# Performance work log

Measured on AMD Instinct MI355X. Metric: run time of the kernel, lower is better.

The kernel has to match this reference:

```python
import jax, jax.numpy as jnp
import numpy as np

N, E, D = 50000, 600000, 128
EPS = 1e-8
BALL_EPS = 1e-5  # keep norms strictly < 1 for artanh


def _logmap0(x):
    # Poincare ball, c=1: logmap0(x) = artanh(||x||) * x / ||x||
    nrm = jnp.linalg.norm(x, axis=-1, keepdims=True)
    nrm_c = jnp.clip(nrm, EPS, 1.0 - BALL_EPS)
    return jnp.arctanh(nrm_c) * x / nrm_c


def _expmap0(v):
    # Poincare ball, c=1: expmap0(v) = tanh(||v||) * v / ||v||
    nrm = jnp.linalg.norm(v, axis=-1, keepdims=True)
    nrm_c = jnp.maximum(nrm, EPS)
    return jnp.tanh(nrm_c) * v / nrm_c


def setup_inputs() -> dict:
    key = jax.random.key(0)
    ks = jax.random.split(key, 7)
    # node features scaled to lie well inside the unit ball (valid Poincare points)
    x = jax.random.normal(ks[0], (N, D), dtype=jnp.float32) * 0.01
    edge_index = jax.random.randint(ks[1], (2, E), 0, N, dtype=jnp.int32)
    s = 1.0 / np.sqrt(D)
    w_msg1 = jax.random.normal(ks[2], (D, D), dtype=jnp.float32) * s
    w_msg2 = jax.random.normal(ks[3], (D, D), dtype=jnp.float32) * s
    w_upd1 = jax.random.normal(ks[4], (D, D), dtype=jnp.float32) * s
    w_upd2 = jax.random.normal(ks[5], (D, D), dtype=jnp.float32) * s
    b = lambda: jnp.zeros((D,), dtype=jnp.float32)
    return {"x": x, "edge_index": edge_index,
            "w_msg1": w_msg1, "b_msg1": b(), "w_msg2": w_msg2, "b_msg2": b(),
            "w_upd1": w_upd1, "b_upd1": b(), "w_upd2": w_upd2, "b_upd2": b()}


def reference(x, edge_index, w_msg1, b_msg1, w_msg2, b_msg2,
              w_upd1, b_upd1, w_upd2, b_upd2):
    x_t = _logmap0(x)                                  # [N, D]
    row, col = edge_index[0], edge_index[1]            # dst, src
    h = x_t[col]                                       # gather [E, D]
    msgs = jax.nn.relu(h @ w_msg1 + b_msg1) @ w_msg2 + b_msg2   # [E, D]
    # mean aggregation: scatter-add then divide by in-degree
    summed = jax.ops.segment_sum(msgs, row, num_segments=N)      # [N, D]
    count = jax.ops.segment_sum(jnp.ones((E,), dtype=jnp.float32), row, num_segments=N)
    out = summed / (count[:, None] + EPS)
    out = jax.nn.relu(out @ w_upd1 + b_upd1) @ w_upd2 + b_upd2
    return _expmap0(out)
```

## Files before the change

kernel.cpp:

```cpp
#include <hip/hip_runtime.h>
#include <hip/hip_bf16.h>


#define DD 128
#define CAP 64

typedef __attribute__((ext_vector_type(8))) short short8;
typedef __attribute__((ext_vector_type(4))) float f32x4;

__device__ __forceinline__ unsigned short f2bf(float f) {
  unsigned u = __float_as_uint(f);
  u += 0x7fffu + ((u >> 16) & 1u);
  return (unsigned short)(u >> 16);
}
__device__ __forceinline__ float bf2f(short h) {
  return __uint_as_float(((unsigned)(unsigned short)h) << 16);
}

__global__ void k_init(const float* __restrict__ w1, const float* __restrict__ w2,
                       const float* __restrict__ w3, const float* __restrict__ w4,
                       unsigned short* __restrict__ P, int* __restrict__ degv, int N) {
  if (blockIdx.x < 32) {
    int idx = blockIdx.x * 256 + threadIdx.x;
    int m = idx >> 11;
    int id = idx & 2047;
    int f = id >> 6, l = id & 63;
    int cc = f >> 2, s = f & 3, q = l >> 4, n15 = l & 15;
    const float* W = (m == 0) ? w1 : (m == 1) ? w2 : (m == 2) ? w3 : w4;
    const float* wp = W + (s * 32 + q * 8) * DD + cc * 16 + n15;
    unsigned short* op = P + (size_t)m * 16384 + (size_t)id * 8;
#pragma unroll
    for (int j = 0; j < 8; ++j) op[j] = f2bf(wp[j * DD]);
  } else {
    int i = (blockIdx.x - 32) * 256 + threadIdx.x;
    if (i < N) degv[i] = 0;
  }
}

__global__ __launch_bounds__(512) void k_stage1(
    const float* __restrict__ x, const int* __restrict__ ei,
    const unsigned short* __restrict__ Pa, const float* __restrict__ ba,
    const unsigned short* __restrict__ Pb, const float* __restrict__ bb,
    unsigned short* __restrict__ node_msg, int* __restrict__ degv,
    int* __restrict__ ebuf, int N, int E, int nf) {
  __shared__ unsigned short As[64 * 136];
  const int tid = threadIdx.x;

  if (blockIdx.x >= nf) {
    int e0 = (blockIdx.x - nf) * 1024 + tid;
    int e1 = e0 + 512;
    int d0 = 0, d1 = 0, s0i = 0, s1i = 0;
    if (e0 < E) { d0 = ei[e0]; s0i = ei[E + e0]; }
    if (e1 < E) { d1 = ei[e1]; s1i = ei[E + e1]; }
    int p0 = 0, p1 = 0;
    if (e0 < E) p0 = atomicAdd(degv + d0, 1);
    if (e1 < E) p1 = atomicAdd(degv + d1, 1);
    if (e0 < E && p0 < CAP) ebuf[(size_t)d0 * CAP + p0] = s0i;
    if (e1 < E && p1 < CAP) ebuf[(size_t)d1 * CAP + p1] = s1i;
    return;
  }

  const int lane = tid & 63;
  const int wv = tid >> 6;
  const int rt = wv >> 1;
  const int ct = wv & 1;
  const int q = lane >> 4;
  const int n15 = lane & 15;
  const int row0 = blockIdx.x * 64;
  const int g = (wv << 2) | q;

#pragma unroll
  for (int i = 0; i < 2; ++i) {
    const int r = g * 2 + i;
    const int grow = row0 + r;
    f32x4 s0 = {0.f, 0.f, 0.f, 0.f}, s1 = {0.f, 0.f, 0.f, 0.f};
    if (grow < N) {
      const f32x4* p = (const f32x4*)(x + (size_t)grow * DD + n15 * 8);
      s0 = p[0];
      s1 = p[1];
      float ss = s0[0]*s0[0] + s0[1]*s0[1] + s0[2]*s0[2] + s0[3]*s0[3]
               + s1[0]*s1[0] + s1[1]*s1[1] + s1[2]*s1[2] + s1[3]*s1[3];
      ss += __shfl_xor(ss, 1);
      ss += __shfl_xor(ss, 2);
      ss += __shfl_xor(ss, 4);
      ss += __shfl_xor(ss, 8);
      float nrm = sqrtf(ss);
      float nc = fminf(fmaxf(nrm, 1e-8f), 1.0f - 1e-5f);
      float sc = atanhf(nc) / nc;
      s0 *= sc;
      s1 *= sc;
    }
    uint4 pk;
    pk.x = (unsigned)f2bf(s0[0]) | ((unsigned)f2bf(s0[1]) << 16);
    pk.y = (unsigned)f2bf(s0[2]) | ((unsigned)f2bf(s0[3]) << 16);
    pk.z = (unsigned)f2bf(s1[0]) | ((unsigned)f2bf(s1[1]) << 16);
    pk.w = (unsigned)f2bf(s1[2]) | ((unsigned)f2bf(s1[3]) << 16);
    *(uint4*)((unsigned*)As + r * 68 + n15 * 4) = pk;
  }
  __syncthreads();

  float bc[4];
#pragma unroll
  for (int c = 0; c < 4; ++c) bc[c] = ba[ct * 64 + c * 16 + n15];
  f32x4 acc[4];
#pragma unroll
  for (int c = 0; c < 4; ++c) acc[c] = (f32x4){0.f, 0.f, 0.f, 0.f};
  const int abase = (rt * 16 + n15) * 136 + q * 8;
#pragma unroll
  for (int s = 0; s < 4; ++s) {
    short8 a = *(const short8*)&As[abase + s * 32];
#pragma unroll
    for (int c = 0; c < 4; ++c) {
      short8 b = *(const short8*)&Pa[(size_t)(((((ct << 2) | c) << 2) | s) * 64 + lane) * 8];
      acc[c] = __builtin_amdgcn_mfma_f32_16x16x32_bf16(a, b, acc[c], 0, 0, 0);
    }
  }
  __syncthreads();

#pragma unroll
  for (int c = 0; c < 4; ++c)
#pragma unroll
    for (int rr = 0; rr < 4; ++rr) {
      float v = fmaxf(acc[c][rr] + bc[c], 0.f);
      As[(rt * 16 + q * 4 + rr) * 136 + ct * 64 + c * 16 + n15] = f2bf(v);
    }
  __syncthreads();

#pragma unroll
  for (int c = 0; c < 4; ++c) bc[c] = bb[ct * 64 + c * 16 + n15];
#pragma unroll
  for (int c = 0; c < 4; ++c) acc[c] = (f32x4){0.f, 0.f, 0.f, 0.f};
#pragma unroll
  for (int s = 0; s < 4; ++s) {
    short8 a = *(const short8*)&As[abase + s * 32];
#pragma unroll
    for (int c = 0; c < 4; ++c) {
      short8 b = *(const short8*)&Pb[(size_t)(((((ct << 2) | c) << 2) | s) * 64 + lane) * 8];
      acc[c] = __builtin_amdgcn_mfma_f32_16x16x32_bf16(a, b, acc[c], 0, 0, 0);
    }
  }

  __syncthreads();
#pragma unroll
  for (int c = 0; c < 4; ++c)
#pragma unroll
    for (int rr = 0; rr < 4; ++rr)
      As[(rt * 16 + q * 4 + rr) * 136 + ct * 64 + c * 16 + n15] =
          f2bf(acc[c][rr] + bc[c]);
  __syncthreads();
#pragma unroll
  for (int k = 0; k < 2; ++k) {
    int u = tid + k * 512;
    int r = u >> 4, ch = u & 15;
    int grow = row0 + r;
    if (grow < N)
      *(short8*)(node_msg + (size_t)grow * DD + ch * 8) =
          *(const short8*)&As[r * 136 + ch * 8];
  }
}

__global__ __launch_bounds__(512) void k_stage2(
    const unsigned short* __restrict__ node_msg, const int* __restrict__ degv,
    const int* __restrict__ ebuf, const unsigned short* __restrict__ Pa,
    const float* __restrict__ ba, const unsigned short* __restrict__ Pb,
    const float* __restrict__ bb, float* __restrict__ out, int N) {
  __shared__ unsigned short As[64 * 136];
  __shared__ float nrmb[128];
  const int tid = threadIdx.x;
  const int lane = tid & 63;
  const int wv = tid >> 6;
  const int rt = wv >> 1;
  const int ct = wv & 1;
  const int q = lane >> 4;
  const int n15 = lane & 15;
  const int row0 = blockIdx.x * 64;
  const int g = (wv << 2) | q;

  int dpre[2];
#pragma unroll
  for (int i = 0; i < 2; ++i) {
    int grow = row0 + g * 2 + i;
    dpre[i] = (grow < N) ? degv[grow] : 0;
  }

#pragma unroll
  for (int i = 0; i < 2; ++i) {
    const int r = g * 2 + i;
    const int grow = row0 + r;
    f32x4 s0 = {0.f, 0.f, 0.f, 0.f}, s1 = {0.f, 0.f, 0.f, 0.f};
    if (grow < N) {
      const int d = dpre[i];
      const int dl = (d < CAP) ? d : CAP;
      const int* eb = ebuf + (size_t)grow * CAP;
      f32x4 t0 = {0.f, 0.f, 0.f, 0.f}, t1 = {0.f, 0.f, 0.f, 0.f};
      int t = 0;
      for (; t + 3 < dl; t += 4) {
        int4 idx = *(const int4*)(eb + t);
        short8 v0 = *(const short8*)(node_msg + (size_t)idx.x * DD + n15 * 8);
        short8 v1 = *(const short8*)(node_msg + (size_t)idx.y * DD + n15 * 8);
        short8 v2 = *(const short8*)(node_msg + (size_t)idx.z * DD + n15 * 8);
        short8 v3 = *(const short8*)(node_msg + (size_t)idx.w * DD + n15 * 8);
#pragma unroll
        for (int j = 0; j < 4; ++j) {
          s0[j] += bf2f(v0[j]) + bf2f(v1[j]);
          s1[j] += bf2f(v0[j + 4]) + bf2f(v1[j + 4]);
          t0[j] += bf2f(v2[j]) + bf2f(v3[j]);
          t1[j] += bf2f(v2[j + 4]) + bf2f(v3[j + 4]);
        }
      }
      for (; t < dl; ++t) {
        int sa = eb[t];
        short8 va = *(const short8*)(node_msg + (size_t)sa * DD + n15 * 8);
#pragma unroll
        for (int j = 0; j < 4; ++j) {
          s0[j] += bf2f(va[j]);
          s1[j] += bf2f(va[j + 4]);
        }
      }
      s0 += t0;
      s1 += t1;
      float inv = 1.f / ((float)d + 1e-8f);
      s0 *= inv;
      s1 *= inv;
    }
    uint4 pk;
    pk.x = (unsigned)f2bf(s0[0]) | ((unsigned)f2bf(s0[1]) << 16);
    pk.y = (unsigned)f2bf(s0[2]) | ((unsigned)f2bf(s0[3]) << 16);
    pk.z = (unsigned)f2bf(s1[0]) | ((unsigned)f2bf(s1[1]) << 16);
    pk.w = (unsigned)f2bf(s1[2]) | ((unsigned)f2bf(s1[3]) << 16);
    *(uint4*)((unsigned*)As + r * 68 + n15 * 4) = pk;
  }
  __syncthreads();

  float bc[4];
#pragma unroll
  for (int c = 0; c < 4; ++c) bc[c] = ba[ct * 64 + c * 16 + n15];
  f32x4 acc[4];
#pragma unroll
  for (int c = 0; c < 4; ++c) acc[c] = (f32x4){0.f, 0.f, 0.f, 0.f};
  const int abase = (rt * 16 + n15) * 136 + q * 8;
#pragma unroll
  for (int s = 0; s < 4; ++s) {
    short8 a = *(const short8*)&As[abase + s * 32];
#pragma unroll
    for (int c = 0; c < 4; ++c) {
      short8 b = *(const short8*)&Pa[(size_t)(((((ct << 2) | c) << 2) | s) * 64 + lane) * 8];
      acc[c] = __builtin_amdgcn_mfma_f32_16x16x32_bf16(a, b, acc[c], 0, 0, 0);
    }
  }
  __syncthreads();

#pragma unroll
  for (int c = 0; c < 4; ++c)
#pragma unroll
    for (int rr = 0; rr < 4; ++rr) {
      float v = fmaxf(acc[c][rr] + bc[c], 0.f);
      As[(rt * 16 + q * 4 + rr) * 136 + ct * 64 + c * 16 + n15] = f2bf(v);
    }
  __syncthreads();

#pragma unroll
  for (int c = 0; c < 4; ++c) bc[c] = bb[ct * 64 + c * 16 + n15];
#pragma unroll
  for (int c = 0; c < 4; ++c) acc[c] = (f32x4){0.f, 0.f, 0.f, 0.f};
#pragma unroll
  for (int s = 0; s < 4; ++s) {
    short8 a = *(const short8*)&As[abase + s * 32];
#pragma unroll
    for (int c = 0; c < 4; ++c) {
      short8 b = *(const short8*)&Pb[(size_t)(((((ct << 2) | c) << 2) | s) * 64 + lane) * 8];
      acc[c] = __builtin_amdgcn_mfma_f32_16x16x32_bf16(a, b, acc[c], 0, 0, 0);
    }
  }

  float v[4][4];
#pragma unroll
  for (int rr = 0; rr < 4; ++rr) {
    float ssq = 0.f;
#pragma unroll
    for (int c = 0; c < 4; ++c) {
      v[c][rr] = acc[c][rr] + bc[c];
      ssq += v[c][rr] * v[c][rr];
    }
    ssq += __shfl_xor(ssq, 1);
    ssq += __shfl_xor(ssq, 2);
    ssq += __shfl_xor(ssq, 4);
    ssq += __shfl_xor(ssq, 8);
    if (n15 == 0) nrmb[(rt * 16 + q * 4 + rr) * 2 + ct] = ssq;
  }
  __syncthreads();
#pragma unroll
  for (int rr = 0; rr < 4; ++rr) {
    int r = rt * 16 + q * 4 + rr;
    int grow = row0 + r;
    float ssq = nrmb[r * 2] + nrmb[r * 2 + 1];
    float nrm = sqrtf(ssq);
    float nc = fmaxf(nrm, 1e-8f);
    float sc = tanhf(nc) / nc;
    if (grow < N) {
#pragma unroll
      for (int c = 0; c < 4; ++c)
        __builtin_nontemporal_store(
            v[c][rr] * sc, out + (size_t)grow * DD + ct * 64 + c * 16 + n15);
    }
  }
}

extern "C" void kernel_launch(void* const* d_in, const int* in_sizes, int n_in,
                              void* d_out, int out_size, void* d_ws, size_t ws_size,
                              hipStream_t stream) {
  const float* x = (const float*)d_in[0];
  const int* ei = (const int*)d_in[1];
  const float* w1 = (const float*)d_in[2];
  const float* b1 = (const float*)d_in[3];
  const float* w2 = (const float*)d_in[4];
  const float* b2 = (const float*)d_in[5];
  const float* w3 = (const float*)d_in[6];
  const float* b3 = (const float*)d_in[7];
  const float* w4 = (const float*)d_in[8];
  const float* b4 = (const float*)d_in[9];
  const int N = in_sizes[0] / DD;
  const int E = in_sizes[1] / 2;
  const int nf = (N + 63) / 64;
  const int ne = (E + 1023) / 1024;

  unsigned short* node_msg = (unsigned short*)d_ws;
  int* degv = (int*)(node_msg + (size_t)N * DD);
  int* ebuf = degv + N;
  uintptr_t pw = (uintptr_t)(ebuf + (size_t)N * CAP);
  pw = (pw + 63) & ~(uintptr_t)63;
  unsigned short* P = (unsigned short*)pw;
  float* outp = (float*)d_out;

  hipLaunchKernelGGL(k_init, dim3(32 + (N + 255) / 256), dim3(256), 0, stream,
                     w1, w2, w3, w4, P, degv, N);
  hipLaunchKernelGGL(k_stage1, dim3(nf + ne), dim3(512), 0, stream,
                     x, ei, P, b1, P + 16384, b2, node_msg, degv, ebuf, N, E, nf);
  hipLaunchKernelGGL(k_stage2, dim3(nf), dim3(512), 0, stream,
                     node_msg, degv, ebuf, P + 2 * 16384, b3, P + 3 * 16384, b4,
                     outp, N);
}
```

Before: 169.1 us.

## Schedule edge-bucketing blocks first and prefetch first 16 neighbor rows in aggregation

Edge-bucketing blocks now come first in the stage-1 grid and each handles 2048 edges, issuing all loads, then all atomics, then all stores. This lets the atomic scatter start early and overlap with the feature transform blocks. In stage 2 the first 16 neighbor indices are loaded as int4 vectors and 16 bf16 message rows are gathered up front, giving more memory-level parallelism before accumulation. The trade-off is higher register pressure and unconditional reads of ebuf slots beyond the node's degree; node 0's row is gathered for unused slots, wasting bandwidth for low-degree nodes.

```diff
diff --git a/kernel.cpp b/kernel.cpp
--- a/kernel.cpp
+++ b/kernel.cpp
@@ -42,21 +42,27 @@
     const unsigned short* __restrict__ Pa, const float* __restrict__ ba,
     const unsigned short* __restrict__ Pb, const float* __restrict__ bb,
     unsigned short* __restrict__ node_msg, int* __restrict__ degv,
-    int* __restrict__ ebuf, int N, int E, int nf) {
+    int* __restrict__ ebuf, int N, int E, int ne) {
   __shared__ unsigned short As[64 * 136];
   const int tid = threadIdx.x;
 
-  if (blockIdx.x >= nf) {
-    int e0 = (blockIdx.x - nf) * 1024 + tid;
-    int e1 = e0 + 512;
-    int d0 = 0, d1 = 0, s0i = 0, s1i = 0;
-    if (e0 < E) { d0 = ei[e0]; s0i = ei[E + e0]; }
-    if (e1 < E) { d1 = ei[e1]; s1i = ei[E + e1]; }
-    int p0 = 0, p1 = 0;
-    if (e0 < E) p0 = atomicAdd(degv + d0, 1);
-    if (e1 < E) p1 = atomicAdd(degv + d1, 1);
-    if (e0 < E && p0 < CAP) ebuf[(size_t)d0 * CAP + p0] = s0i;
-    if (e1 < E && p1 < CAP) ebuf[(size_t)d1 * CAP + p1] = s1i;
+  if (blockIdx.x < ne) {
+    int eb_[4], d_[4], s_[4], p_[4];
+#pragma unroll
+    for (int k = 0; k < 4; ++k) {
+      int e = blockIdx.x * 2048 + k * 512 + tid;
+      eb_[k] = e;
+      if (e < E) {
+        d_[k] = ei[e];
+        s_[k] = ei[E + e];
+      }
+    }
+#pragma unroll
+    for (int k = 0; k < 4; ++k)
+      if (eb_[k] < E) p_[k] = atomicAdd(degv + d_[k], 1);
+#pragma unroll
+    for (int k = 0; k < 4; ++k)
+      if (eb_[k] < E && p_[k] < CAP) ebuf[(size_t)d_[k] * CAP + p_[k]] = s_[k];
     return;
   }
 
@@ -66,7 +72,7 @@
   const int ct = wv & 1;
   const int q = lane >> 4;
   const int n15 = lane & 15;
-  const int row0 = blockIdx.x * 64;
+  const int row0 = (blockIdx.x - ne) * 64;
   const int g = (wv << 2) | q;
 
 #pragma unroll
@@ -192,8 +198,35 @@
       const int d = dpre[i];
       const int dl = (d < CAP) ? d : CAP;
       const int* eb = ebuf + (size_t)grow * CAP;
+      int4 cA = *(const int4*)(eb);
+      int4 cB = *(const int4*)(eb + 4);
+      int4 cC = *(const int4*)(eb + 8);
+      int4 cD = *(const int4*)(eb + 12);
+      int id[16] = {cA.x, cA.y, cA.z, cA.w, cB.x, cB.y, cB.z, cB.w,
+                    cC.x, cC.y, cC.z, cC.w, cD.x, cD.y, cD.z, cD.w};
+      short8 v[16];
+#pragma unroll
+      for (int t = 0; t < 16; ++t) {
+        int sidx = (t < dl) ? id[t] : 0;
+        v[t] = *(const short8*)(node_msg + (size_t)sidx * DD + n15 * 8);
+      }
       f32x4 t0 = {0.f, 0.f, 0.f, 0.f}, t1 = {0.f, 0.f, 0.f, 0.f};
-      int t = 0;
+#pragma unroll
+      for (int t = 0; t < 16; ++t) {
+        if (t < dl) {
+#pragma unroll
+          for (int j = 0; j < 4; ++j) {
+            if (t & 1) {
+              t0[j] += bf2f(v[t][j]);
+              t1[j] += bf2f(v[t][j + 4]);
+            } else {
+              s0[j] += bf2f(v[t][j]);
+              s1[j] += bf2f(v[t][j + 4]);
+            }
+          }
+        }
+      }
+      int t = 16;
       for (; t + 3 < dl; t += 4) {
         int4 idx = *(const int4*)(eb + t);
         short8 v0 = *(const short8*)(node_msg + (size_t)idx.x * DD + n15 * 8);
@@ -322,7 +355,7 @@
   const int N = in_sizes[0] / DD;
   const int E = in_sizes[1] / 2;
   const int nf = (N + 63) / 64;
-  const int ne = (E + 1023) / 1024;
+  const int ne = (E + 2047) / 2048;
 
   unsigned short* node_msg = (unsigned short*)d_ws;
   int* degv = (int*)(node_msg + (size_t)N * DD);
@@ -334,8 +367,8 @@
 
   hipLaunchKernelGGL(k_init, dim3(32 + (N + 255) / 256), dim3(256), 0, stream,
                      w1, w2, w3, w4, P, degv, N);
-  hipLaunchKernelGGL(k_stage1, dim3(nf + ne), dim3(512), 0, stream,
-                     x, ei, P, b1, P + 16384, b2, node_msg, degv, ebuf, N, E, nf);
+  hipLaunchKernelGGL(k_stage1, dim3(ne + nf), dim3(512), 0, stream,
+                     x, ei, P, b1, P + 16384, b2, node_msg, degv, ebuf, N, E, ne);
   hipLaunchKernelGGL(k_stage2, dim3(nf), dim3(512), 0, stream,
                      node_msg, degv, ebuf, P + 2 * 16384, b3, P + 3 * 16384, b4,
                      outp, N);
```

Result: no change. 167.8 us (median of 2 runs) (-0.8%).
